# Optimization experiments

Measured on AMD Instinct MI355X. Metric: run time of the kernel, lower is better.

The kernel has to match this reference:

```python
import jax, jax.numpy as jnp
import numpy as np

B, T, D, N = 2, 2048, 1024, 16
DT_RANK = 64  # ceil(D / 16)


def setup_inputs() -> dict:
    key = jax.random.key(0)
    ks = jax.random.split(key, 8)
    x = jax.random.normal(ks[0], (B, T, D), dtype=jnp.float32)
    # Linear weights stored as (out, in) like torch; applied as x @ W.T
    W_B = jax.random.normal(ks[1], (N, D), dtype=jnp.float32) / np.sqrt(D)
    W_C = jax.random.normal(ks[2], (N, D), dtype=jnp.float32) / np.sqrt(D)
    W_dt1 = jax.random.normal(ks[3], (DT_RANK, D), dtype=jnp.float32) / np.sqrt(D)
    W_dt2 = jax.random.normal(ks[4], (D, DT_RANK), dtype=jnp.float32) / np.sqrt(DT_RANK)
    # dt bias init: inverse-softplus of dt sampled log-uniform in [dt_min, dt_max]
    dt_min, dt_max = 1e-3, 1e-1
    u = jax.random.uniform(ks[5], (D,), dtype=jnp.float32)
    dt_init = jnp.clip(jnp.exp(u * (np.log(dt_max) - np.log(dt_min)) + np.log(dt_min)), 1e-4, None)
    b_dt2 = dt_init + jnp.log(-jnp.expm1(-dt_init))
    # log_A: per original non-HiPPO path, A in (0.5, 1.0), broadcast to (D, N)
    a = jax.random.uniform(ks[6], (N,), dtype=jnp.float32) * 0.5 + 0.5
    log_A = jnp.broadcast_to(jnp.log(a)[None, :], (D, N)).copy()
    D_skip = jnp.ones((D,), dtype=jnp.float32)
    return {"x": x, "W_B": W_B, "W_C": W_C, "W_dt1": W_dt1,
            "W_dt2": W_dt2, "b_dt2": b_dt2, "log_A": log_A, "D_skip": D_skip}


def _selective_scan(A_bar, B_bar, C):
    # A_bar, B_bar: (B, T, D, N); C: (B, T, N) -> y: (B, T, D)
    def step(h, inputs):
        a_t, b_t, c_t = inputs  # (B,D,N), (B,D,N), (B,N)
        h = a_t * h + b_t
        y_t = jnp.einsum('bdn,bn->bd', h, c_t)
        return h, y_t

    h0 = jnp.zeros(A_bar.shape[:1] + A_bar.shape[2:], dtype=A_bar.dtype)  # (B,D,N)
    xs = (jnp.moveaxis(A_bar, 1, 0), jnp.moveaxis(B_bar, 1, 0), jnp.moveaxis(C, 1, 0))
    _, ys = jax.lax.scan(step, h0, xs)  # ys: (T, B, D)
    return jnp.moveaxis(ys, 0, 1)


def reference(x, W_B, W_C, W_dt1, W_dt2, b_dt2, log_A, D_skip):
    # Projections
    B_t = jnp.einsum('btd,nd->btn', x, W_B)          # (B,T,N)
    C_t = jnp.einsum('btd,nd->btn', x, W_C)          # (B,T,N)
    dt_raw = jnp.einsum('btr,dr->btd', jnp.einsum('btd,rd->btr', x, W_dt1), W_dt2) + b_dt2
    dt = jax.nn.softplus(dt_raw)                     # (B,T,D)
    A = -jnp.exp(log_A)                              # (D,N), negative
    # Discretization
    A_bar = jnp.exp(dt[..., None] * A[None, None])   # (B,T,D,N)
    dB = (A_bar - 1.0) / (A[None, None] + 1e-8)
    B_bar = dB * x[..., None] * B_t[:, :, None, :]   # (B,T,D,N)
    y = _selective_scan(A_bar, B_bar, C_t)           # (B,T,D)
    return y + D_skip * x
```

## Files before the change

kernel.cpp:

```cpp
#include <hip/hip_runtime.h>
#include <hip/hip_bf16.h>

#define BB 2
#define TT 2048
#define DD 1024
#define NN 16
#define RR 64
#define MM (BB*TT)
#define KDIM DD
#define CHUNK 32
#define NCHUNK (TT/CHUNK)
#define KSPLIT 8

#define BT_OFF 0
#define CT_OFF 65536
#define R1_OFF 131072
#define DT_OFF 393216
#define P_OFF  4587520
#define S_OFF  6684672
#define H_OFF  8781824
#define PP_OFF 10878976

#define LOG2E 1.4426950408889634f

#if __has_builtin(__builtin_amdgcn_exp2f)
#define EXP2(x) __builtin_amdgcn_exp2f(x)
#else
#define EXP2(x) exp2f(x)
#endif

__device__ __forceinline__ float softplus_f(float z) {
    return fmaxf(z, 0.0f) + log1pf(expf(-fabsf(z)));
}

__global__ __launch_bounds__(256) void k_proj96(
    const float* __restrict__ x, const float* __restrict__ W_B,
    const float* __restrict__ W_C, const float* __restrict__ W_dt1,
    float* __restrict__ Pp)
{
    __shared__ float xs[16][68];
    __shared__ float wsT[16][97];

    const int tid = threadIdx.x;
    const int r0 = blockIdx.x * 64;
    const int kbase = blockIdx.y * (KDIM / KSPLIT);
    const int tx = tid & 15;
    const int ty = tid >> 4;

    float acc[4][6];
    #pragma unroll
    for (int i = 0; i < 4; i++)
        #pragma unroll
        for (int j = 0; j < 6; j++) acc[i][j] = 0.0f;

    for (int kc = 0; kc < KDIM / KSPLIT; kc += 16) {
        {
            const int row = tid >> 2;
            const int kq = (tid & 3) * 4;
            float4 v = *(const float4*)(x + (size_t)(r0 + row) * KDIM + kbase + kc + kq);
            xs[kq + 0][row] = v.x; xs[kq + 1][row] = v.y;
            xs[kq + 2][row] = v.z; xs[kq + 3][row] = v.w;
        }
        #pragma unroll
        for (int i = 0; i < 6; i++) {
            const int idx = i * 256 + tid;
            const int c = idx >> 4;
            const int kk = idx & 15;
            const float* wrow; int cc;
            if (c < 16)      { wrow = W_B;   cc = c; }
            else if (c < 32) { wrow = W_C;   cc = c - 16; }
            else             { wrow = W_dt1; cc = c - 32; }
            wsT[kk][c] = wrow[(size_t)cc * KDIM + kbase + kc + kk];
        }
        __syncthreads();
        #pragma unroll
        for (int kk = 0; kk < 16; kk++) {
            const float a0 = xs[kk][ty * 4 + 0];
            const float a1 = xs[kk][ty * 4 + 1];
            const float a2 = xs[kk][ty * 4 + 2];
            const float a3 = xs[kk][ty * 4 + 3];
            #pragma unroll
            for (int j = 0; j < 6; j++) {
                const float b = wsT[kk][tx + j * 16];
                acc[0][j] = fmaf(a0, b, acc[0][j]);
                acc[1][j] = fmaf(a1, b, acc[1][j]);
                acc[2][j] = fmaf(a2, b, acc[2][j]);
                acc[3][j] = fmaf(a3, b, acc[3][j]);
            }
        }
        __syncthreads();
    }

    float* out = Pp + (size_t)blockIdx.y * (MM * 96);
    #pragma unroll
    for (int i = 0; i < 4; i++) {
        const int r = r0 + ty * 4 + i;
        #pragma unroll
        for (int j = 0; j < 6; j++)
            out[(size_t)r * 96 + tx + j * 16] = acc[i][j];
    }
}

__global__ __launch_bounds__(256) void k_reduce96(
    const float* __restrict__ Pp, const float* __restrict__ log_A,
    float* __restrict__ Bt, float* __restrict__ Ct, float* __restrict__ R1)
{
    const int gid = blockIdx.x * 256 + threadIdx.x;
    const int e0 = gid * 4;
    float4 s = *(const float4*)(Pp + e0);
    #pragma unroll
    for (int p = 1; p < KSPLIT; p++) {
        const float4 v = *(const float4*)(Pp + (size_t)p * MM * 96 + e0);
        s.x += v.x; s.y += v.y; s.z += v.z; s.w += v.w;
    }
    const int r = e0 / 96;
    const int c = e0 - r * 96;
    if (c < 16) {
        const float4 lgj = *(const float4*)(log_A + c);
        s.x *= 1.0f / (-__expf(lgj.x) + 1e-8f);
        s.y *= 1.0f / (-__expf(lgj.y) + 1e-8f);
        s.z *= 1.0f / (-__expf(lgj.z) + 1e-8f);
        s.w *= 1.0f / (-__expf(lgj.w) + 1e-8f);
        *(float4*)(Bt + (size_t)r * NN + c) = s;
    } else if (c < 32) {
        *(float4*)(Ct + (size_t)r * NN + (c - 16)) = s;
    } else {
        *(float4*)(R1 + (size_t)r * RR + (c - 32)) = s;
    }
}

__global__ __launch_bounds__(256) void k_dtproj(
    const float* __restrict__ R1, const float* __restrict__ W_dt2,
    const float* __restrict__ b_dt2, float* __restrict__ dt)
{
    __shared__ float r1s[64][68];
    __shared__ float wsT[64][128];

    const int tid = threadIdx.x;
    const int r0 = blockIdx.x * 64;
    const int d0 = blockIdx.y * 128;

    #pragma unroll
    for (int i = 0; i < 4; i++) {
        const int f = tid + i * 256;
        const int row = f >> 4;
        const int kq = (f & 15) * 4;
        *(float4*)&r1s[row][kq] = *(const float4*)(R1 + (size_t)(r0 + row) * RR + kq);
    }
    {
        const int dl = tid >> 1;
        const int khalf = (tid & 1) * 32;
        const float* src = W_dt2 + (size_t)(d0 + dl) * RR + khalf;
        #pragma unroll
        for (int kq = 0; kq < 32; kq += 4) {
            const float4 v = *(const float4*)(src + kq);
            wsT[khalf + kq + 0][dl] = v.x;
            wsT[khalf + kq + 1][dl] = v.y;
            wsT[khalf + kq + 2][dl] = v.z;
            wsT[khalf + kq + 3][dl] = v.w;
        }
    }
    __syncthreads();

    const int cg = tid & 15;
    const int rg = tid >> 4;

    float4 acc[4][2];
    #pragma unroll
    for (int i = 0; i < 4; i++) {
        acc[i][0] = make_float4(0.f, 0.f, 0.f, 0.f);
        acc[i][1] = make_float4(0.f, 0.f, 0.f, 0.f);
    }

    for (int k4 = 0; k4 < 16; k4++) {
        float r1a[4][4];
        #pragma unroll
        for (int i = 0; i < 4; i++) {
            const float4 v = *(const float4*)&r1s[rg * 4 + i][k4 * 4];
            r1a[i][0] = v.x; r1a[i][1] = v.y; r1a[i][2] = v.z; r1a[i][3] = v.w;
        }
        #pragma unroll
        for (int kk = 0; kk < 4; kk++) {
            const int k = k4 * 4 + kk;
            const float4 w0 = *(const float4*)&wsT[k][cg * 4];
            const float4 w1 = *(const float4*)&wsT[k][64 + cg * 4];
            #pragma unroll
            for (int i = 0; i < 4; i++) {
                const float a = r1a[i][kk];
                acc[i][0].x = fmaf(a, w0.x, acc[i][0].x);
                acc[i][0].y = fmaf(a, w0.y, acc[i][0].y);
                acc[i][0].z = fmaf(a, w0.z, acc[i][0].z);
                acc[i][0].w = fmaf(a, w0.w, acc[i][0].w);
                acc[i][1].x = fmaf(a, w1.x, acc[i][1].x);
                acc[i][1].y = fmaf(a, w1.y, acc[i][1].y);
                acc[i][1].z = fmaf(a, w1.z, acc[i][1].z);
                acc[i][1].w = fmaf(a, w1.w, acc[i][1].w);
            }
        }
    }

    #pragma unroll
    for (int q = 0; q < 2; q++) {
        const float4 bias = *(const float4*)(b_dt2 + d0 + q * 64 + cg * 4);
        #pragma unroll
        for (int i = 0; i < 4; i++) {
            const int row = r0 + rg * 4 + i;
            float4 o;
            o.x = softplus_f(acc[i][q].x + bias.x);
            o.y = softplus_f(acc[i][q].y + bias.y);
            o.z = softplus_f(acc[i][q].z + bias.z);
            o.w = softplus_f(acc[i][q].w + bias.w);
            *(float4*)(dt + (size_t)row * DD + d0 + q * 64 + cg * 4) = o;
        }
    }
}

__global__ __launch_bounds__(256, 2) void k_scan1(
    const float* __restrict__ x, const float* __restrict__ dt,
    const float* __restrict__ Bt, const float* __restrict__ log_A,
    float* __restrict__ P, float* __restrict__ Sg)
{
    __shared__ float bt_s[CHUNK][NN];

    const int tid = threadIdx.x;
    const int d = blockIdx.x * 256 + tid;
    const int c = blockIdx.y;
    const int b = blockIdx.z;
    const int base = b * TT + c * CHUNK;

    if (tid < CHUNK * NN / 4) {
        const int t = tid >> 2;
        const int jc = (tid & 3) * 4;
        *(float4*)&bt_s[t][jc] = *(const float4*)(Bt + (size_t)(base + t) * NN + jc);
    }

    float A2[16];
    #pragma unroll
    for (int q = 0; q < 4; q++) {
        const float4 lg = *(const float4*)(log_A + d * NN + q * 4);
        A2[q * 4 + 0] = -__expf(lg.x) * LOG2E;
        A2[q * 4 + 1] = -__expf(lg.y) * LOG2E;
        A2[q * 4 + 2] = -__expf(lg.z) * LOG2E;
        A2[q * 4 + 3] = -__expf(lg.w) * LOG2E;
    }

    const float* gdt = dt + (size_t)base * DD + d;
    const float* gx  = x  + (size_t)base * DD + d;

    __syncthreads();

    float s[16];
    #pragma unroll
    for (int n = 0; n < 16; n++) s[n] = 0.0f;
    float dtsum = 0.0f;

    #pragma unroll 4
    for (int t = 0; t < CHUNK; t++) {
        const float dtv = gdt[(size_t)t * DD];
        const float xv  = gx[(size_t)t * DD];
        dtsum += dtv;
        #pragma unroll
        for (int q = 0; q < 4; q++) {
            const float4 bt4 = *(const float4*)&bt_s[t][q * 4];
            const float a0 = EXP2(dtv * A2[q * 4 + 0]);
            const float a1 = EXP2(dtv * A2[q * 4 + 1]);
            const float a2 = EXP2(dtv * A2[q * 4 + 2]);
            const float a3 = EXP2(dtv * A2[q * 4 + 3]);
            const float u0 = xv * bt4.x;
            const float u1 = xv * bt4.y;
            const float u2 = xv * bt4.z;
            const float u3 = xv * bt4.w;
            s[q * 4 + 0] = fmaf(a0, s[q * 4 + 0] + u0, -u0);
            s[q * 4 + 1] = fmaf(a1, s[q * 4 + 1] + u1, -u1);
            s[q * 4 + 2] = fmaf(a2, s[q * 4 + 2] + u2, -u2);
            s[q * 4 + 3] = fmaf(a3, s[q * 4 + 3] + u3, -u3);
        }
    }

    const size_t o = ((size_t)(c * BB + b) * DD + d) * NN;
    #pragma unroll
    for (int q = 0; q < 4; q++) {
        *(float4*)(P + o + q * 4) = make_float4(
            EXP2(A2[q * 4 + 0] * dtsum), EXP2(A2[q * 4 + 1] * dtsum),
            EXP2(A2[q * 4 + 2] * dtsum), EXP2(A2[q * 4 + 3] * dtsum));
        *(float4*)(Sg + o + q * 4) = make_float4(
            s[q * 4 + 0], s[q * 4 + 1], s[q * 4 + 2], s[q * 4 + 3]);
    }
}

__global__ __launch_bounds__(256) void k_comb(
    const float* __restrict__ P, const float* __restrict__ Sg,
    float* __restrict__ Hs)
{
    const int flat = blockIdx.x * 256 + threadIdx.x;
    float h = 0.0f;
    #pragma unroll 8
    for (int c = 0; c < NCHUNK; c++) {
        const size_t idx = (size_t)c * (BB * DD * NN) + flat;
        Hs[idx] = h;
        h = fmaf(P[idx], h, Sg[idx]);
    }
}

__global__ __launch_bounds__(256, 2) void k_scan2(
    const float* __restrict__ x, const float* __restrict__ dt,
    const float* __restrict__ Bt, const float* __restrict__ Ct,
    const float* __restrict__ log_A, const float* __restrict__ D_skip,
    const float* __restrict__ Hs, float* __restrict__ y)
{
    __shared__ float bt_s[CHUNK][NN];
    __shared__ float ct_s[CHUNK][NN];

    const int tid = threadIdx.x;
    const int d = blockIdx.x * 256 + tid;
    const int c = blockIdx.y;
    const int b = blockIdx.z;
    const int base = b * TT + c * CHUNK;

    if (tid < 128) {
        const int t = tid >> 2;
        const int jc = (tid & 3) * 4;
        *(float4*)&bt_s[t][jc] = *(const float4*)(Bt + (size_t)(base + t) * NN + jc);
    } else {
        const int t2 = (tid - 128) >> 2;
        const int jc = (tid & 3) * 4;
        *(float4*)&ct_s[t2][jc] = *(const float4*)(Ct + (size_t)(base + t2) * NN + jc);
    }

    float A2[16];
    #pragma unroll
    for (int q = 0; q < 4; q++) {
        const float4 lg = *(const float4*)(log_A + d * NN + q * 4);
        A2[q * 4 + 0] = -__expf(lg.x) * LOG2E;
        A2[q * 4 + 1] = -__expf(lg.y) * LOG2E;
        A2[q * 4 + 2] = -__expf(lg.z) * LOG2E;
        A2[q * 4 + 3] = -__expf(lg.w) * LOG2E;
    }
    const float dsk = D_skip[d];

    float h[16];
    {
        const size_t hoff = (size_t)c * (BB * DD * NN) + (size_t)b * (DD * NN) + (size_t)d * NN;
        #pragma unroll
        for (int q = 0; q < 4; q++) {
            const float4 hv = *(const float4*)(Hs + hoff + q * 4);
            h[q * 4 + 0] = hv.x; h[q * 4 + 1] = hv.y;
            h[q * 4 + 2] = hv.z; h[q * 4 + 3] = hv.w;
        }
    }

    const float* gdt = dt + (size_t)base * DD + d;
    const float* gx  = x  + (size_t)base * DD + d;

    __syncthreads();

    float* yp = y + (size_t)base * DD + d;

    #pragma unroll 4
    for (int t = 0; t < CHUNK; t++) {
        const float dtv = gdt[(size_t)t * DD];
        const float xv  = gx[(size_t)t * DD];
        float part = 0.0f;
        #pragma unroll
        for (int q = 0; q < 4; q++) {
            const float4 bt4 = *(const float4*)&bt_s[t][q * 4];
            const float4 ct4 = *(const float4*)&ct_s[t][q * 4];
            const float a0 = EXP2(dtv * A2[q * 4 + 0]);
            const float a1 = EXP2(dtv * A2[q * 4 + 1]);
            const float a2 = EXP2(dtv * A2[q * 4 + 2]);
            const float a3 = EXP2(dtv * A2[q * 4 + 3]);
            const float u0 = xv * bt4.x;
            const float u1 = xv * bt4.y;
            const float u2 = xv * bt4.z;
            const float u3 = xv * bt4.w;
            h[q * 4 + 0] = fmaf(a0, h[q * 4 + 0] + u0, -u0);
            h[q * 4 + 1] = fmaf(a1, h[q * 4 + 1] + u1, -u1);
            h[q * 4 + 2] = fmaf(a2, h[q * 4 + 2] + u2, -u2);
            h[q * 4 + 3] = fmaf(a3, h[q * 4 + 3] + u3, -u3);
            part = fmaf(h[q * 4 + 0], ct4.x, part);
            part = fmaf(h[q * 4 + 1], ct4.y, part);
            part = fmaf(h[q * 4 + 2], ct4.z, part);
            part = fmaf(h[q * 4 + 3], ct4.w, part);
        }
        yp[(size_t)t * DD] = fmaf(dsk, xv, part);
    }
}

extern "C" void kernel_launch(void* const* d_in, const int* in_sizes, int n_in,
                              void* d_out, int out_size, void* d_ws, size_t ws_size,
                              hipStream_t stream)
{
    const float* x      = (const float*)d_in[0];
    const float* W_B    = (const float*)d_in[1];
    const float* W_C    = (const float*)d_in[2];
    const float* W_dt1  = (const float*)d_in[3];
    const float* W_dt2  = (const float*)d_in[4];
    const float* b_dt2  = (const float*)d_in[5];
    const float* log_A  = (const float*)d_in[6];
    const float* D_skip = (const float*)d_in[7];
    float* y = (float*)d_out;

    float* ws = (float*)d_ws;
    float* Bt = ws + BT_OFF;
    float* Ct = ws + CT_OFF;
    float* R1 = ws + R1_OFF;
    float* dt = ws + DT_OFF;
    float* P  = ws + P_OFF;
    float* S  = ws + S_OFF;
    float* Hs = ws + H_OFF;
    float* Pp = ws + PP_OFF;

    k_proj96<<<dim3(MM / 64, KSPLIT), 256, 0, stream>>>(x, W_B, W_C, W_dt1, Pp);
    k_reduce96<<<dim3(MM * 96 / 4 / 256), 256, 0, stream>>>(Pp, log_A, Bt, Ct, R1);
    k_dtproj<<<dim3(MM / 64, DD / 128), 256, 0, stream>>>(R1, W_dt2, b_dt2, dt);
    k_scan1<<<dim3(DD / 256, NCHUNK, BB), 256, 0, stream>>>(x, dt, Bt, log_A, P, S);
    k_comb<<<dim3(BB * DD * NN / 256), 256, 0, stream>>>(P, S, Hs);
    k_scan2<<<dim3(DD / 256, NCHUNK, BB), 256, 0, stream>>>(x, dt, Bt, Ct, log_A, D_skip, Hs, y);
}
```

Measured before the change: 168.4 us.

## Fuse dt projection and softplus into both scan kernels, drop dt buffer

Removes the separate dt projection kernel and recomputes dt = softplus(R1 · W_dt2 + b) inside both scan passes. Each thread keeps its 64-wide W_dt2 row in registers, and the chunk's R1 rows are staged in shared memory. This avoids writing and then twice reading the 16 MB dt intermediate, and saves one launch. In exchange the dt projection is computed twice (64 FMAs per timestep per thread in each pass), register pressure rises, and the launch bounds drop the minimum-blocks hint.

```diff
diff --git a/kernel.cpp b/kernel.cpp
--- a/kernel.cpp
+++ b/kernel.cpp
@@ -129,98 +129,14 @@
     }
 }
 
-__global__ __launch_bounds__(256) void k_dtproj(
-    const float* __restrict__ R1, const float* __restrict__ W_dt2,
-    const float* __restrict__ b_dt2, float* __restrict__ dt)
-{
-    __shared__ float r1s[64][68];
-    __shared__ float wsT[64][128];
-
-    const int tid = threadIdx.x;
-    const int r0 = blockIdx.x * 64;
-    const int d0 = blockIdx.y * 128;
-
-    #pragma unroll
-    for (int i = 0; i < 4; i++) {
-        const int f = tid + i * 256;
-        const int row = f >> 4;
-        const int kq = (f & 15) * 4;
-        *(float4*)&r1s[row][kq] = *(const float4*)(R1 + (size_t)(r0 + row) * RR + kq);
-    }
-    {
-        const int dl = tid >> 1;
-        const int khalf = (tid & 1) * 32;
-        const float* src = W_dt2 + (size_t)(d0 + dl) * RR + khalf;
-        #pragma unroll
-        for (int kq = 0; kq < 32; kq += 4) {
-            const float4 v = *(const float4*)(src + kq);
-            wsT[khalf + kq + 0][dl] = v.x;
-            wsT[khalf + kq + 1][dl] = v.y;
-            wsT[khalf + kq + 2][dl] = v.z;
-            wsT[khalf + kq + 3][dl] = v.w;
-        }
-    }
-    __syncthreads();
-
-    const int cg = tid & 15;
-    const int rg = tid >> 4;
-
-    float4 acc[4][2];
-    #pragma unroll
-    for (int i = 0; i < 4; i++) {
-        acc[i][0] = make_float4(0.f, 0.f, 0.f, 0.f);
-        acc[i][1] = make_float4(0.f, 0.f, 0.f, 0.f);
-    }
-
-    for (int k4 = 0; k4 < 16; k4++) {
-        float r1a[4][4];
-        #pragma unroll
-        for (int i = 0; i < 4; i++) {
-            const float4 v = *(const float4*)&r1s[rg * 4 + i][k4 * 4];
-            r1a[i][0] = v.x; r1a[i][1] = v.y; r1a[i][2] = v.z; r1a[i][3] = v.w;
-        }
-        #pragma unroll
-        for (int kk = 0; kk < 4; kk++) {
-            const int k = k4 * 4 + kk;
-            const float4 w0 = *(const float4*)&wsT[k][cg * 4];
-            const float4 w1 = *(const float4*)&wsT[k][64 + cg * 4];
-            #pragma unroll
-            for (int i = 0; i < 4; i++) {
-                const float a = r1a[i][kk];
-                acc[i][0].x = fmaf(a, w0.x, acc[i][0].x);
-                acc[i][0].y = fmaf(a, w0.y, acc[i][0].y);
-                acc[i][0].z = fmaf(a, w0.z, acc[i][0].z);
-                acc[i][0].w = fmaf(a, w0.w, acc[i][0].w);
-                acc[i][1].x = fmaf(a, w1.x, acc[i][1].x);
-                acc[i][1].y = fmaf(a, w1.y, acc[i][1].y);
-                acc[i][1].z = fmaf(a, w1.z, acc[i][1].z);
-                acc[i][1].w = fmaf(a, w1.w, acc[i][1].w);
-            }
-        }
-    }
-
-    #pragma unroll
-    for (int q = 0; q < 2; q++) {
-        const float4 bias = *(const float4*)(b_dt2 + d0 + q * 64 + cg * 4);
-        #pragma unroll
-        for (int i = 0; i < 4; i++) {
-            const int row = r0 + rg * 4 + i;
-            float4 o;
-            o.x = softplus_f(acc[i][q].x + bias.x);
-            o.y = softplus_f(acc[i][q].y + bias.y);
-            o.z = softplus_f(acc[i][q].z + bias.z);
-            o.w = softplus_f(acc[i][q].w + bias.w);
-            *(float4*)(dt + (size_t)row * DD + d0 + q * 64 + cg * 4) = o;
-        }
-    }
-}
-
-__global__ __launch_bounds__(256, 2) void k_scan1(
-    const float* __restrict__ x, const float* __restrict__ dt,
+__global__ __launch_bounds__(256) void k_scan1(
+    const float* __restrict__ x, const float* __restrict__ R1,
+    const float* __restrict__ W_dt2, const float* __restrict__ b_dt2,
     const float* __restrict__ Bt, const float* __restrict__ log_A,
     float* __restrict__ P, float* __restrict__ Sg)
 {
     __shared__ float bt_s[CHUNK][NN];
+    __shared__ float r1s[CHUNK][RR];
 
     const int tid = threadIdx.x;
     const int d = blockIdx.x * 256 + tid;
@@ -228,11 +144,24 @@
     const int b = blockIdx.z;
     const int base = b * TT + c * CHUNK;
 
+    #pragma unroll
+    for (int i = 0; i < 2; i++) {
+        const int f = tid + i * 256;
+        const int row = f >> 4;
+        const int kq = (f & 15) * 4;
+        *(float4*)&r1s[row][kq] = *(const float4*)(R1 + (size_t)(base + row) * RR + kq);
+    }
     if (tid < CHUNK * NN / 4) {
         const int t = tid >> 2;
         const int jc = (tid & 3) * 4;
         *(float4*)&bt_s[t][jc] = *(const float4*)(Bt + (size_t)(base + t) * NN + jc);
     }
+
+    float4 w4[16];
+    #pragma unroll
+    for (int q = 0; q < 16; q++)
+        w4[q] = *(const float4*)(W_dt2 + (size_t)d * RR + q * 4);
+    const float bias = b_dt2[d];
 
     float A2[16];
     #pragma unroll
@@ -244,8 +173,7 @@
         A2[q * 4 + 3] = -__expf(lg.w) * LOG2E;
     }
 
-    const float* gdt = dt + (size_t)base * DD + d;
-    const float* gx  = x  + (size_t)base * DD + d;
+    const float* gx = x + (size_t)base * DD + d;
 
     __syncthreads();
 
@@ -254,9 +182,25 @@
     for (int n = 0; n < 16; n++) s[n] = 0.0f;
     float dtsum = 0.0f;
 
-    #pragma unroll 4
+    #pragma unroll 2
     for (int t = 0; t < CHUNK; t++) {
-        const float dtv = gdt[(size_t)t * DD];
+        float pa0 = bias, pa1 = 0.f, pa2 = 0.f, pa3 = 0.f;
+        #pragma unroll
+        for (int q = 0; q < 16; q += 4) {
+            const float4 r0v = *(const float4*)&r1s[t][(q + 0) * 4];
+            const float4 r1v = *(const float4*)&r1s[t][(q + 1) * 4];
+            const float4 r2v = *(const float4*)&r1s[t][(q + 2) * 4];
+            const float4 r3v = *(const float4*)&r1s[t][(q + 3) * 4];
+            pa0 = fmaf(r0v.x, w4[q + 0].x, pa0); pa0 = fmaf(r0v.y, w4[q + 0].y, pa0);
+            pa0 = fmaf(r0v.z, w4[q + 0].z, pa0); pa0 = fmaf(r0v.w, w4[q + 0].w, pa0);
+            pa1 = fmaf(r1v.x, w4[q + 1].x, pa1); pa1 = fmaf(r1v.y, w4[q + 1].y, pa1);
+            pa1 = fmaf(r1v.z, w4[q + 1].z, pa1); pa1 = fmaf(r1v.w, w4[q + 1].w, pa1);
+            pa2 = fmaf(r2v.x, w4[q + 2].x, pa2); pa2 = fmaf(r2v.y, w4[q + 2].y, pa2);
+            pa2 = fmaf(r2v.z, w4[q + 2].z, pa2); pa2 = fmaf(r2v.w, w4[q + 2].w, pa2);
+            pa3 = fmaf(r3v.x, w4[q + 3].x, pa3); pa3 = fmaf(r3v.y, w4[q + 3].y, pa3);
+            pa3 = fmaf(r3v.z, w4[q + 3].z, pa3); pa3 = fmaf(r3v.w, w4[q + 3].w, pa3);
+        }
+        const float dtv = softplus_f((pa0 + pa1) + (pa2 + pa3));
         const float xv  = gx[(size_t)t * DD];
         dtsum += dtv;
         #pragma unroll
@@ -302,14 +246,16 @@
     }
 }
 
-__global__ __launch_bounds__(256, 2) void k_scan2(
-    const float* __restrict__ x, const float* __restrict__ dt,
+__global__ __launch_bounds__(256) void k_scan2(
+    const float* __restrict__ x, const float* __restrict__ R1,
+    const float* __restrict__ W_dt2, const float* __restrict__ b_dt2,
     const float* __restrict__ Bt, const float* __restrict__ Ct,
     const float* __restrict__ log_A, const float* __restrict__ D_skip,
     const float* __restrict__ Hs, float* __restrict__ y)
 {
     __shared__ float bt_s[CHUNK][NN];
     __shared__ float ct_s[CHUNK][NN];
+    __shared__ float r1s[CHUNK][RR];
 
     const int tid = threadIdx.x;
     const int d = blockIdx.x * 256 + tid;
@@ -317,6 +263,13 @@
     const int b = blockIdx.z;
     const int base = b * TT + c * CHUNK;
 
+    #pragma unroll
+    for (int i = 0; i < 2; i++) {
+        const int f = tid + i * 256;
+        const int row = f >> 4;
+        const int kq = (f & 15) * 4;
+        *(float4*)&r1s[row][kq] = *(const float4*)(R1 + (size_t)(base + row) * RR + kq);
+    }
     if (tid < 128) {
         const int t = tid >> 2;
         const int jc = (tid & 3) * 4;
@@ -327,6 +280,12 @@
         *(float4*)&ct_s[t2][jc] = *(const float4*)(Ct + (size_t)(base + t2) * NN + jc);
     }
 
+    float4 w4[16];
+    #pragma unroll
+    for (int q = 0; q < 16; q++)
+        w4[q] = *(const float4*)(W_dt2 + (size_t)d * RR + q * 4);
+    const float bias = b_dt2[d];
+
     float A2[16];
     #pragma unroll
     for (int q = 0; q < 4; q++) {
@@ -349,16 +308,31 @@
         }
     }
 
-    const float* gdt = dt + (size_t)base * DD + d;
-    const float* gx  = x  + (size_t)base * DD + d;
+    const float* gx = x + (size_t)base * DD + d;
 
     __syncthreads();
 
     float* yp = y + (size_t)base * DD + d;
 
-    #pragma unroll 4
+    #pragma unroll 2
     for (int t = 0; t < CHUNK; t++) {
-        const float dtv = gdt[(size_t)t * DD];
+        float pa0 = bias, pa1 = 0.f, pa2 = 0.f, pa3 = 0.f;
+        #pragma unroll
+        for (int q = 0; q < 16; q += 4) {
+            const float4 r0v = *(const float4*)&r1s[t][(q + 0) * 4];
+            const float4 r1v = *(const float4*)&r1s[t][(q + 1) * 4];
+            const float4 r2v = *(const float4*)&r1s[t][(q + 2) * 4];
+            const float4 r3v = *(const float4*)&r1s[t][(q + 3) * 4];
+            pa0 = fmaf(r0v.x, w4[q + 0].x, pa0); pa0 = fmaf(r0v.y, w4[q + 0].y, pa0);
+            pa0 = fmaf(r0v.z, w4[q + 0].z, pa0); pa0 = fmaf(r0v.w, w4[q + 0].w, pa0);
+            pa1 = fmaf(r1v.x, w4[q + 1].x, pa1); pa1 = fmaf(r1v.y, w4[q + 1].y, pa1);
+            pa1 = fmaf(r1v.z, w4[q + 1].z, pa1); pa1 = fmaf(r1v.w, w4[q + 1].w, pa1);
+            pa2 = fmaf(r2v.x, w4[q + 2].x, pa2); pa2 = fmaf(r2v.y, w4[q + 2].y, pa2);
+            pa2 = fmaf(r2v.z, w4[q + 2].z, pa2); pa2 = fmaf(r2v.w, w4[q + 2].w, pa2);
+            pa3 = fmaf(r3v.x, w4[q + 3].x, pa3); pa3 = fmaf(r3v.y, w4[q + 3].y, pa3);
+            pa3 = fmaf(r3v.z, w4[q + 3].z, pa3); pa3 = fmaf(r3v.w, w4[q + 3].w, pa3);
+        }
+        const float dtv = softplus_f((pa0 + pa1) + (pa2 + pa3));
         const float xv  = gx[(size_t)t * DD];
         float part = 0.0f;
         #pragma unroll
@@ -404,7 +378,6 @@
     float* Bt = ws + BT_OFF;
     float* Ct = ws + CT_OFF;
     float* R1 = ws + R1_OFF;
-    float* dt = ws + DT_OFF;
     float* P  = ws + P_OFF;
     float* S  = ws + S_OFF;
     float* Hs = ws + H_OFF;
@@ -412,8 +385,7 @@
 
     k_proj96<<<dim3(MM / 64, KSPLIT), 256, 0, stream>>>(x, W_B, W_C, W_dt1, Pp);
     k_reduce96<<<dim3(MM * 96 / 4 / 256), 256, 0, stream>>>(Pp, log_A, Bt, Ct, R1);
-    k_dtproj<<<dim3(MM / 64, DD / 128), 256, 0, stream>>>(R1, W_dt2, b_dt2, dt);
-    k_scan1<<<dim3(DD / 256, NCHUNK, BB), 256, 0, stream>>>(x, dt, Bt, log_A, P, S);
+    k_scan1<<<dim3(DD / 256, NCHUNK, BB), 256, 0, stream>>>(x, R1, W_dt2, b_dt2, Bt, log_A, P, S);
     k_comb<<<dim3(BB * DD * NN / 256), 256, 0, stream>>>(P, S, Hs);
-    k_scan2<<<dim3(DD / 256, NCHUNK, BB), 256, 0, stream>>>(x, dt, Bt, Ct, log_A, D_skip, Hs, y);
-}
+    k_scan2<<<dim3(DD / 256, NCHUNK, BB), 256, 0, stream>>>(x, R1, W_dt2, b_dt2, Bt, Ct, log_A, D_skip, Hs, y);
+}
```

After: 204.7 us. +21.6%, slower.
